# Performance work log

Measured on AMD Instinct MI355X. Metric: run time of the kernel, lower is better.

## Reference

```python
import jax, jax.numpy as jnp
import numpy as np

NHID = 1024
NOUT = 50257
NLAY = 1
MAX_LEN = 24


def setup_inputs() -> dict:
    key = jax.random.key(0)
    ks = jax.random.split(key, 16)
    s = 0.02
    return {
        "inp": jax.random.randint(ks[0], (1,), 0, NOUT),
        "hidden": jax.random.normal(ks[1], (1, 1, NHID), dtype=jnp.float32),
        "encoder_output": jax.random.normal(ks[2], (1, NHID), dtype=jnp.float32),
        "encoder_outputs": jax.random.normal(ks[3], (MAX_LEN, NHID), dtype=jnp.float32),
        "emb_W": jax.random.normal(ks[4], (NOUT, NHID), dtype=jnp.float32) * s,
        "attn_W": jax.random.normal(ks[5], (MAX_LEN, 2 * NHID), dtype=jnp.float32) * s,
        "attn_b": jnp.zeros((MAX_LEN,), dtype=jnp.float32),
        "comb_W": jax.random.normal(ks[6], (NHID, 2 * NHID), dtype=jnp.float32) * s,
        "comb_b": jnp.zeros((NHID,), dtype=jnp.float32),
        "W_ih": jax.random.normal(ks[7], (3 * NHID, NHID), dtype=jnp.float32) * s,
        "W_hh": jax.random.normal(ks[8], (3 * NHID, NHID), dtype=jnp.float32) * s,
        "b_ih": jnp.zeros((3 * NHID,), dtype=jnp.float32),
        "b_hh": jnp.zeros((3 * NHID,), dtype=jnp.float32),
        "out_W": jax.random.normal(ks[9], (NOUT, NHID), dtype=jnp.float32) * s,
        "out_b": jnp.zeros((NOUT,), dtype=jnp.float32),
    }


def reference(inp, hidden, encoder_output, encoder_outputs, emb_W, attn_W, attn_b,
              comb_W, comb_b, W_ih, W_hh, b_ih, b_hh, out_W, out_b):
    # embedding lookup (dropout is identity in eval); [1, nhid]
    embedded = emb_W[inp]
    h = hidden[0]  # [1, nhid]
    # Bahdanau-style attention over encoder_outputs [max_len, nhid]
    attn_in = jnp.concatenate([embedded, h], axis=1)            # [1, 2*nhid]
    attn_weights = jax.nn.softmax(attn_in @ attn_W.T + attn_b, axis=-1)  # [1, max_len]
    attn_applied = attn_weights @ encoder_outputs               # [1, nhid]
    out = jnp.concatenate([embedded, attn_applied], axis=1) @ comb_W.T + comb_b  # [1, nhid]
    # nlay repeated (relu -> GRU step) with the same single-layer GRU weights
    for _ in range(NLAY):
        x = jax.nn.relu(out)
        gi = x @ W_ih.T + b_ih   # [1, 3*nhid]
        gh = h @ W_hh.T + b_hh   # [1, 3*nhid]
        ir, iz, i_n = jnp.split(gi, 3, axis=1)
        hr, hz, h_n = jnp.split(gh, 3, axis=1)
        r = jax.nn.sigmoid(ir + hr)
        z = jax.nn.sigmoid(iz + hz)
        n = jnp.tanh(i_n + r * h_n)
        h = (1.0 - z) * n + z * h
        out = h
    logp = jax.nn.log_softmax(out @ out_W.T + out_b, axis=-1)   # [1, nout]
    return (logp, h[None, :, :], attn_weights)
```

## Files before the change

kernel.cpp:

```cpp
#include <hip/hip_runtime.h>
#include <math.h>

#define NHID 1024
#define NOUT 50257
#define MAXLEN 24

#define WS_APP   0
#define WS_X     1024
#define WS_GH    2048
#define WS_H     5120
#define WS_LOGIT 8192
#define WS_PAIRS 61440

#define LOG_BLOCKS 786

__device__ __forceinline__ float wave_reduce_sum(float v) {
    #pragma unroll
    for (int off = 32; off > 0; off >>= 1) v += __shfl_down(v, off, 64);
    return v;
}

__device__ __forceinline__ void lse_merge(float& m, float& s, float m2, float s2) {
    float M = fmaxf(m, m2);
    s = s * expf(m - M) + s2 * expf(m2 - M);
    m = M;
}

__global__ __launch_bounds__(1024) void
k_attn_gh(const int* __restrict__ inp, const float* __restrict__ hid,
          const float* __restrict__ enc, const float* __restrict__ embW,
          const float* __restrict__ attnW, const float* __restrict__ attnb,
          const float* __restrict__ Whh, const float* __restrict__ bhh,
          float* __restrict__ ws, float* __restrict__ out) {
    const int tid = threadIdx.x;
    const int lane = tid & 63, wave = tid >> 6;
    const float4* hid4 = (const float4*)hid;

    if (blockIdx.x > 0) {
        const int row = (blockIdx.x - 1) * 16 + wave;
        const float4* w4 = (const float4*)(Whh + (size_t)row * NHID);
        float acc = 0.f;
        #pragma unroll
        for (int it = 0; it < 4; ++it) {
            int idx = it * 64 + lane;
            float4 w = w4[idx], h = hid4[idx];
            acc += w.x * h.x + w.y * h.y + w.z * h.z + w.w * h.w;
        }
        acc = wave_reduce_sum(acc);
        if (lane == 0) ws[WS_GH + row] = acc + bhh[row];
        return;
    }

    __shared__ float s_sc[MAXLEN];
    __shared__ float s_w[MAXLEN];
    const float4* emb4 = (const float4*)(embW + (size_t)inp[0] * NHID);
    for (int i = wave; i < MAXLEN; i += 16) {
        const float4* w4 = (const float4*)(attnW + (size_t)i * 2 * NHID);
        float acc = 0.f;
        #pragma unroll
        for (int it = 0; it < 8; ++it) {
            int idx = it * 64 + lane;
            float4 w = w4[idx];
            float4 a = (idx < 256) ? emb4[idx] : hid4[idx - 256];
            acc += w.x * a.x + w.y * a.y + w.z * a.z + w.w * a.w;
        }
        acc = wave_reduce_sum(acc);
        if (lane == 0) s_sc[i] = acc + attnb[i];
    }
    __syncthreads();
    if (tid == 0) {
        float m = -1e30f;
        for (int i = 0; i < MAXLEN; ++i) m = fmaxf(m, s_sc[i]);
        float s = 0.f;
        for (int i = 0; i < MAXLEN; ++i) { float e = expf(s_sc[i] - m); s_w[i] = e; s += e; }
        float inv = 1.f / s;
        for (int i = 0; i < MAXLEN; ++i) { s_w[i] *= inv; out[NOUT + NHID + i] = s_w[i]; }
    }
    __syncthreads();
    {
        float acc = 0.f;
        #pragma unroll 4
        for (int i = 0; i < MAXLEN; ++i) acc += s_w[i] * enc[i * NHID + tid];
        ws[WS_APP + tid] = acc;
    }
}

__global__ __launch_bounds__(256) void
k_comb(const int* __restrict__ inp, const float* __restrict__ embW,
       const float* __restrict__ combW, const float* __restrict__ combb,
       float* __restrict__ ws) {
    const int j = blockIdx.x, t = threadIdx.x;
    const float4* emb4 = (const float4*)(embW + (size_t)inp[0] * NHID);
    const float4* app4 = (const float4*)(ws + WS_APP);
    const float4* w4 = (const float4*)(combW + (size_t)j * 2 * NHID);
    float4 wa = w4[t],       xa = emb4[t];
    float4 wb = w4[256 + t], xb = app4[t];
    float p = wa.x * xa.x + wa.y * xa.y + wa.z * xa.z + wa.w * xa.w
            + wb.x * xb.x + wb.y * xb.y + wb.z * xb.z + wb.w * xb.w;
    p = wave_reduce_sum(p);
    __shared__ float s_r[4];
    if ((t & 63) == 0) s_r[t >> 6] = p;
    __syncthreads();
    if (t == 0) ws[WS_X + j] = fmaxf(s_r[0] + s_r[1] + s_r[2] + s_r[3] + combb[j], 0.f);
}

__global__ __launch_bounds__(256) void
k_gru(const float* __restrict__ hid, const float* __restrict__ Wih,
      const float* __restrict__ bih, float* __restrict__ ws,
      float* __restrict__ out) {
    const int j = blockIdx.x, t = threadIdx.x;
    const float4* x4 = (const float4*)(ws + WS_X);
    float4 xv = x4[t];
    float p[3];
    #pragma unroll
    for (int r = 0; r < 3; ++r) {
        float4 wv = ((const float4*)(Wih + (size_t)(r * NHID + j) * NHID))[t];
        p[r] = wv.x * xv.x + wv.y * xv.y + wv.z * xv.z + wv.w * xv.w;
    }
    __shared__ float s_r[3][4];
    #pragma unroll
    for (int r = 0; r < 3; ++r) {
        float v = wave_reduce_sum(p[r]);
        if ((t & 63) == 0) s_r[r][t >> 6] = v;
    }
    __syncthreads();
    if (t == 0) {
        float gi[3];
        #pragma unroll
        for (int r = 0; r < 3; ++r) gi[r] = s_r[r][0] + s_r[r][1] + s_r[r][2] + s_r[r][3] + bih[r * NHID + j];
        float hr = ws[WS_GH + j], hz = ws[WS_GH + NHID + j], hn = ws[WS_GH + 2 * NHID + j];
        float r_ = 1.f / (1.f + expf(-(gi[0] + hr)));
        float z_ = 1.f / (1.f + expf(-(gi[1] + hz)));
        float n_ = tanhf(gi[2] + r_ * hn);
        float hnew = (1.f - z_) * n_ + z_ * hid[j];
        ws[WS_H + j] = hnew;
        out[NOUT + j] = hnew;
    }
}

__global__ __launch_bounds__(1024) void
k_logits(const float* __restrict__ outW, const float* __restrict__ outb,
         float* __restrict__ ws) {
    const int tid = threadIdx.x;
    const int lane = tid & 63, wave = tid >> 6;
    const float4* h4 = (const float4*)(ws + WS_H);
    float4 hv[4];
    #pragma unroll
    for (int it = 0; it < 4; ++it) hv[it] = h4[it * 64 + lane];
    float m = -1e30f, s = 0.f;
    const int rowBase = blockIdx.x * 64 + wave * 4;
    #pragma unroll
    for (int rr = 0; rr < 4; ++rr) {
        const int row = rowBase + rr;
        if (row >= NOUT) break;
        const float4* w4 = (const float4*)(outW + (size_t)row * NHID);
        float acc = 0.f;
        #pragma unroll
        for (int it = 0; it < 4; ++it) {
            float4 w = w4[it * 64 + lane];
            acc += w.x * hv[it].x + w.y * hv[it].y + w.z * hv[it].z + w.w * hv[it].w;
        }
        acc = wave_reduce_sum(acc);
        if (lane == 0) {
            float v = acc + outb[row];
            ws[WS_LOGIT + row] = v;
            lse_merge(m, s, v, 1.f);
        }
    }
    __shared__ float sm[16], ss[16];
    if (lane == 0) { sm[wave] = m; ss[wave] = s; }
    __syncthreads();
    if (tid == 0) {
        float M = sm[0], S = ss[0];
        #pragma unroll
        for (int w = 1; w < 16; ++w) lse_merge(M, S, sm[w], ss[w]);
        ws[WS_PAIRS + 2 * blockIdx.x] = M;
        ws[WS_PAIRS + 2 * blockIdx.x + 1] = S;
    }
}

__global__ __launch_bounds__(1024) void
k_finalize(const float* __restrict__ ws, float* __restrict__ out) {
    const int tid = threadIdx.x;
    const int lane = tid & 63, wave = tid >> 6;
    float m = -1e30f, s = 0.f;
    if (tid < LOG_BLOCKS) { m = ws[WS_PAIRS + 2 * tid]; s = ws[WS_PAIRS + 2 * tid + 1]; }
    #pragma unroll
    for (int off = 32; off > 0; off >>= 1) {
        float m2 = __shfl_down(m, off, 64);
        float s2 = __shfl_down(s, off, 64);
        lse_merge(m, s, m2, s2);
    }
    __shared__ float sm[16], ss[16];
    __shared__ float sC;
    if (lane == 0) { sm[wave] = m; ss[wave] = s; }
    __syncthreads();
    if (tid == 0) {
        float M = sm[0], S = ss[0];
        #pragma unroll
        for (int w = 1; w < 16; ++w) lse_merge(M, S, sm[w], ss[w]);
        sC = M + logf(S);
    }
    __syncthreads();
    const float C = sC;
    const int i = blockIdx.x * 1024 + tid;
    if (i < NOUT) out[i] = ws[WS_LOGIT + i] - C;
}

extern "C" void kernel_launch(void* const* d_in, const int* in_sizes, int n_in,
                              void* d_out, int out_size, void* d_ws, size_t ws_size,
                              hipStream_t stream) {
    const int*   inp   = (const int*)d_in[0];
    const float* hid   = (const float*)d_in[1];
    const float* enc   = (const float*)d_in[3];
    const float* embW  = (const float*)d_in[4];
    const float* attnW = (const float*)d_in[5];
    const float* attnb = (const float*)d_in[6];
    const float* combW = (const float*)d_in[7];
    const float* combb = (const float*)d_in[8];
    const float* Wih   = (const float*)d_in[9];
    const float* Whh   = (const float*)d_in[10];
    const float* bih   = (const float*)d_in[11];
    const float* bhh   = (const float*)d_in[12];
    const float* outW  = (const float*)d_in[13];
    const float* outb  = (const float*)d_in[14];
    float* out = (float*)d_out;
    float* ws  = (float*)d_ws;

    hipLaunchKernelGGL(k_attn_gh, dim3(1 + 192), dim3(1024), 0, stream,
                       inp, hid, enc, embW, attnW, attnb, Whh, bhh, ws, out);
    hipLaunchKernelGGL(k_comb, dim3(NHID), dim3(256), 0, stream,
                       inp, embW, combW, combb, ws);
    hipLaunchKernelGGL(k_gru, dim3(NHID), dim3(256), 0, stream,
                       hid, Wih, bih, ws, out);
    hipLaunchKernelGGL(k_logits, dim3(LOG_BLOCKS), dim3(1024), 0, stream,
                       outW, outb, ws);
    hipLaunchKernelGGL(k_finalize, dim3(50), dim3(1024), 0, stream,
                       ws, out);
}
```

Baseline: 426.5 us.

## Fuse decoder step into one cooperative persistent kernel with grid syncs

Replaces the five separate kernel launches (attention/gh, combine, GRU, logits, finalize) with a single cooperative kernel of 256 blocks that separates stages with grid-wide syncs. This removes inter-kernel launch gaps and tail effects. The combine and GRU matvecs are remapped to one wave per output row, and the logits stage loops over row groups persistently. The trade-off is fewer resident waves per CU for the bandwidth-bound output projection, plus the cost of grid barriers.

```diff
diff --git a/kernel.cpp b/kernel.cpp
--- a/kernel.cpp
+++ b/kernel.cpp
@@ -1,5 +1,8 @@
 #include <hip/hip_runtime.h>
+#include <hip/hip_cooperative_groups.h>
 #include <math.h>
+
+namespace cg = cooperative_groups;
 
 #define NHID 1024
 #define NOUT 50257
@@ -12,7 +15,8 @@
 #define WS_LOGIT 8192
 #define WS_PAIRS 61440
 
-#define LOG_BLOCKS 786
+#define NBLK 256
+#define NGROUP 786
 
 __device__ __forceinline__ float wave_reduce_sum(float v) {
     #pragma unroll
@@ -27,17 +31,57 @@
 }
 
 __global__ __launch_bounds__(1024) void
-k_attn_gh(const int* __restrict__ inp, const float* __restrict__ hid,
-          const float* __restrict__ enc, const float* __restrict__ embW,
-          const float* __restrict__ attnW, const float* __restrict__ attnb,
-          const float* __restrict__ Whh, const float* __restrict__ bhh,
-          float* __restrict__ ws, float* __restrict__ out) {
+k_fused(const int* __restrict__ inp, const float* __restrict__ hid,
+        const float* __restrict__ enc, const float* __restrict__ embW,
+        const float* __restrict__ attnW, const float* __restrict__ attnb,
+        const float* __restrict__ combW, const float* __restrict__ combb,
+        const float* __restrict__ Wih, const float* __restrict__ Whh,
+        const float* __restrict__ bih, const float* __restrict__ bhh,
+        const float* __restrict__ outW, const float* __restrict__ outb,
+        float* __restrict__ ws, float* __restrict__ out) {
+    cg::grid_group grid = cg::this_grid();
     const int tid = threadIdx.x;
     const int lane = tid & 63, wave = tid >> 6;
+    const int bid = blockIdx.x;
+    const int gwave = bid * 16 + wave;
+
+    __shared__ float s_sc[MAXLEN], s_w[MAXLEN];
+    __shared__ float sm[16], ss[16];
+    __shared__ float sC;
+
     const float4* hid4 = (const float4*)hid;
-
-    if (blockIdx.x > 0) {
-        const int row = (blockIdx.x - 1) * 16 + wave;
+    const float4* emb4 = (const float4*)(embW + (size_t)inp[0] * NHID);
+
+    if (bid == 0) {
+        for (int i = wave; i < MAXLEN; i += 16) {
+            const float4* w4 = (const float4*)(attnW + (size_t)i * 2 * NHID);
+            float acc = 0.f;
+            #pragma unroll
+            for (int it = 0; it < 8; ++it) {
+                int idx = it * 64 + lane;
+                float4 w = w4[idx];
+                float4 a = (idx < 256) ? emb4[idx] : hid4[idx - 256];
+                acc += w.x * a.x + w.y * a.y + w.z * a.z + w.w * a.w;
+            }
+            acc = wave_reduce_sum(acc);
+            if (lane == 0) s_sc[i] = acc + attnb[i];
+        }
+        __syncthreads();
+        if (tid == 0) {
+            float m = -1e30f;
+            for (int i = 0; i < MAXLEN; ++i) m = fmaxf(m, s_sc[i]);
+            float s = 0.f;
+            for (int i = 0; i < MAXLEN; ++i) { float e = expf(s_sc[i] - m); s_w[i] = e; s += e; }
+            float inv = 1.f / s;
+            for (int i = 0; i < MAXLEN; ++i) { s_w[i] *= inv; out[NOUT + NHID + i] = s_w[i]; }
+        }
+        __syncthreads();
+        float acc = 0.f;
+        #pragma unroll 4
+        for (int i = 0; i < MAXLEN; ++i) acc += s_w[i] * enc[i * NHID + tid];
+        ws[WS_APP + tid] = acc;
+    } else if (bid <= 192) {
+        const int row = (bid - 1) * 16 + wave;
         const float4* w4 = (const float4*)(Whh + (size_t)row * NHID);
         float acc = 0.f;
         #pragma unroll
@@ -48,163 +92,119 @@
         }
         acc = wave_reduce_sum(acc);
         if (lane == 0) ws[WS_GH + row] = acc + bhh[row];
-        return;
-    }
-
-    __shared__ float s_sc[MAXLEN];
-    __shared__ float s_w[MAXLEN];
-    const float4* emb4 = (const float4*)(embW + (size_t)inp[0] * NHID);
-    for (int i = wave; i < MAXLEN; i += 16) {
-        const float4* w4 = (const float4*)(attnW + (size_t)i * 2 * NHID);
+    }
+    grid.sync();
+
+    if (gwave < NHID) {
+        const int j = gwave;
+        const float4* app4 = (const float4*)(ws + WS_APP);
+        const float4* w4 = (const float4*)(combW + (size_t)j * 2 * NHID);
         float acc = 0.f;
         #pragma unroll
         for (int it = 0; it < 8; ++it) {
             int idx = it * 64 + lane;
             float4 w = w4[idx];
-            float4 a = (idx < 256) ? emb4[idx] : hid4[idx - 256];
+            float4 a = (idx < 256) ? emb4[idx] : app4[idx - 256];
             acc += w.x * a.x + w.y * a.y + w.z * a.z + w.w * a.w;
         }
         acc = wave_reduce_sum(acc);
-        if (lane == 0) s_sc[i] = acc + attnb[i];
-    }
-    __syncthreads();
-    if (tid == 0) {
-        float m = -1e30f;
-        for (int i = 0; i < MAXLEN; ++i) m = fmaxf(m, s_sc[i]);
-        float s = 0.f;
-        for (int i = 0; i < MAXLEN; ++i) { float e = expf(s_sc[i] - m); s_w[i] = e; s += e; }
-        float inv = 1.f / s;
-        for (int i = 0; i < MAXLEN; ++i) { s_w[i] *= inv; out[NOUT + NHID + i] = s_w[i]; }
+        if (lane == 0) ws[WS_X + j] = fmaxf(acc + combb[j], 0.f);
+    }
+    grid.sync();
+
+    if (gwave < NHID) {
+        const int j = gwave;
+        const float4* x4 = (const float4*)(ws + WS_X);
+        float4 xv[4];
+        #pragma unroll
+        for (int it = 0; it < 4; ++it) xv[it] = x4[it * 64 + lane];
+        float gi[3];
+        #pragma unroll
+        for (int r = 0; r < 3; ++r) {
+            const float4* w4 = (const float4*)(Wih + (size_t)(r * NHID + j) * NHID);
+            float acc = 0.f;
+            #pragma unroll
+            for (int it = 0; it < 4; ++it) {
+                float4 w = w4[it * 64 + lane];
+                acc += w.x * xv[it].x + w.y * xv[it].y + w.z * xv[it].z + w.w * xv[it].w;
+            }
+            gi[r] = wave_reduce_sum(acc);
+        }
+        if (lane == 0) {
+            float ir = gi[0] + bih[j],            hr = ws[WS_GH + j];
+            float iz = gi[1] + bih[NHID + j],     hz = ws[WS_GH + NHID + j];
+            float in_ = gi[2] + bih[2 * NHID + j], hn = ws[WS_GH + 2 * NHID + j];
+            float r_ = 1.f / (1.f + expf(-(ir + hr)));
+            float z_ = 1.f / (1.f + expf(-(iz + hz)));
+            float n_ = tanhf(in_ + r_ * hn);
+            float hnew = (1.f - z_) * n_ + z_ * hid[j];
+            ws[WS_H + j] = hnew;
+            out[NOUT + j] = hnew;
+        }
+    }
+    grid.sync();
+
+    {
+        const float4* h4 = (const float4*)(ws + WS_H);
+        float4 hv[4];
+        #pragma unroll
+        for (int it = 0; it < 4; ++it) hv[it] = h4[it * 64 + lane];
+        float m = -1e30f, s = 0.f;
+        for (int g = bid; g < NGROUP; g += NBLK) {
+            const int rowBase = g * 64 + wave * 4;
+            #pragma unroll
+            for (int rr = 0; rr < 4; ++rr) {
+                const int row = rowBase + rr;
+                if (row < NOUT) {
+                    const float4* w4 = (const float4*)(outW + (size_t)row * NHID);
+                    float acc = 0.f;
+                    #pragma unroll
+                    for (int it = 0; it < 4; ++it) {
+                        float4 w = w4[it * 64 + lane];
+                        acc += w.x * hv[it].x + w.y * hv[it].y + w.z * hv[it].z + w.w * hv[it].w;
+                    }
+                    acc = wave_reduce_sum(acc);
+                    if (lane == 0) {
+                        float v = acc + outb[row];
+                        ws[WS_LOGIT + row] = v;
+                        lse_merge(m, s, v, 1.f);
+                    }
+                }
+            }
+        }
+        if (lane == 0) { sm[wave] = m; ss[wave] = s; }
+        __syncthreads();
+        if (tid == 0) {
+            float M = sm[0], S = ss[0];
+            #pragma unroll
+            for (int w = 1; w < 16; ++w) lse_merge(M, S, sm[w], ss[w]);
+            ws[WS_PAIRS + 2 * bid] = M;
+            ws[WS_PAIRS + 2 * bid + 1] = S;
+        }
+    }
+    grid.sync();
+
+    if (wave == 0) {
+        float m = -1e30f, s = 0.f;
+        #pragma unroll
+        for (int k = 0; k < 4; ++k) {
+            int idx = k * 64 + lane;
+            lse_merge(m, s, ws[WS_PAIRS + 2 * idx], ws[WS_PAIRS + 2 * idx + 1]);
+        }
+        #pragma unroll
+        for (int off = 32; off > 0; off >>= 1) {
+            float m2 = __shfl_down(m, off, 64);
+            float s2 = __shfl_down(s, off, 64);
+            lse_merge(m, s, m2, s2);
+        }
+        if (lane == 0) sC = m + logf(s);
     }
     __syncthreads();
     {
-        float acc = 0.f;
-        #pragma unroll 4
-        for (int i = 0; i < MAXLEN; ++i) acc += s_w[i] * enc[i * NHID + tid];
-        ws[WS_APP + tid] = acc;
-    }
-}
-
-__global__ __launch_bounds__(256) void
-k_comb(const int* __restrict__ inp, const float* __restrict__ embW,
-       const float* __restrict__ combW, const float* __restrict__ combb,
-       float* __restrict__ ws) {
-    const int j = blockIdx.x, t = threadIdx.x;
-    const float4* emb4 = (const float4*)(embW + (size_t)inp[0] * NHID);
-    const float4* app4 = (const float4*)(ws + WS_APP);
-    const float4* w4 = (const float4*)(combW + (size_t)j * 2 * NHID);
-    float4 wa = w4[t],       xa = emb4[t];
-    float4 wb = w4[256 + t], xb = app4[t];
-    float p = wa.x * xa.x + wa.y * xa.y + wa.z * xa.z + wa.w * xa.w
-            + wb.x * xb.x + wb.y * xb.y + wb.z * xb.z + wb.w * xb.w;
-    p = wave_reduce_sum(p);
-    __shared__ float s_r[4];
-    if ((t & 63) == 0) s_r[t >> 6] = p;
-    __syncthreads();
-    if (t == 0) ws[WS_X + j] = fmaxf(s_r[0] + s_r[1] + s_r[2] + s_r[3] + combb[j], 0.f);
-}
-
-__global__ __launch_bounds__(256) void
-k_gru(const float* __restrict__ hid, const float* __restrict__ Wih,
-      const float* __restrict__ bih, float* __restrict__ ws,
-      float* __restrict__ out) {
-    const int j = blockIdx.x, t = threadIdx.x;
-    const float4* x4 = (const float4*)(ws + WS_X);
-    float4 xv = x4[t];
-    float p[3];
-    #pragma unroll
-    for (int r = 0; r < 3; ++r) {
-        float4 wv = ((const float4*)(Wih + (size_t)(r * NHID + j) * NHID))[t];
-        p[r] = wv.x * xv.x + wv.y * xv.y + wv.z * xv.z + wv.w * xv.w;
-    }
-    __shared__ float s_r[3][4];
-    #pragma unroll
-    for (int r = 0; r < 3; ++r) {
-        float v = wave_reduce_sum(p[r]);
-        if ((t & 63) == 0) s_r[r][t >> 6] = v;
-    }
-    __syncthreads();
-    if (t == 0) {
-        float gi[3];
-        #pragma unroll
-        for (int r = 0; r < 3; ++r) gi[r] = s_r[r][0] + s_r[r][1] + s_r[r][2] + s_r[r][3] + bih[r * NHID + j];
-        float hr = ws[WS_GH + j], hz = ws[WS_GH + NHID + j], hn = ws[WS_GH + 2 * NHID + j];
-        float r_ = 1.f / (1.f + expf(-(gi[0] + hr)));
-        float z_ = 1.f / (1.f + expf(-(gi[1] + hz)));
-        float n_ = tanhf(gi[2] + r_ * hn);
-        float hnew = (1.f - z_) * n_ + z_ * hid[j];
-        ws[WS_H + j] = hnew;
-        out[NOUT + j] = hnew;
-    }
-}
-
-__global__ __launch_bounds__(1024) void
-k_logits(const float* __restrict__ outW, const float* __restrict__ outb,
-         float* __restrict__ ws) {
-    const int tid = threadIdx.x;
-    const int lane = tid & 63, wave = tid >> 6;
-    const float4* h4 = (const float4*)(ws + WS_H);
-    float4 hv[4];
-    #pragma unroll
-    for (int it = 0; it < 4; ++it) hv[it] = h4[it * 64 + lane];
-    float m = -1e30f, s = 0.f;
-    const int rowBase = blockIdx.x * 64 + wave * 4;
-    #pragma unroll
-    for (int rr = 0; rr < 4; ++rr) {
-        const int row = rowBase + rr;
-        if (row >= NOUT) break;
-        const float4* w4 = (const float4*)(outW + (size_t)row * NHID);
-        float acc = 0.f;
-        #pragma unroll
-        for (int it = 0; it < 4; ++it) {
-            float4 w = w4[it * 64 + lane];
-            acc += w.x * hv[it].x + w.y * hv[it].y + w.z * hv[it].z + w.w * hv[it].w;
-        }
-        acc = wave_reduce_sum(acc);
-        if (lane == 0) {
-            float v = acc + outb[row];
-            ws[WS_LOGIT + row] = v;
-            lse_merge(m, s, v, 1.f);
-        }
-    }
-    __shared__ float sm[16], ss[16];
-    if (lane == 0) { sm[wave] = m; ss[wave] = s; }
-    __syncthreads();
-    if (tid == 0) {
-        float M = sm[0], S = ss[0];
-        #pragma unroll
-        for (int w = 1; w < 16; ++w) lse_merge(M, S, sm[w], ss[w]);
-        ws[WS_PAIRS + 2 * blockIdx.x] = M;
-        ws[WS_PAIRS + 2 * blockIdx.x + 1] = S;
-    }
-}
-
-__global__ __launch_bounds__(1024) void
-k_finalize(const float* __restrict__ ws, float* __restrict__ out) {
-    const int tid = threadIdx.x;
-    const int lane = tid & 63, wave = tid >> 6;
-    float m = -1e30f, s = 0.f;
-    if (tid < LOG_BLOCKS) { m = ws[WS_PAIRS + 2 * tid]; s = ws[WS_PAIRS + 2 * tid + 1]; }
-    #pragma unroll
-    for (int off = 32; off > 0; off >>= 1) {
-        float m2 = __shfl_down(m, off, 64);
-        float s2 = __shfl_down(s, off, 64);
-        lse_merge(m, s, m2, s2);
-    }
-    __shared__ float sm[16], ss[16];
-    __shared__ float sC;
-    if (lane == 0) { sm[wave] = m; ss[wave] = s; }
-    __syncthreads();
-    if (tid == 0) {
-        float M = sm[0], S = ss[0];
-        #pragma unroll
-        for (int w = 1; w < 16; ++w) lse_merge(M, S, sm[w], ss[w]);
-        sC = M + logf(S);
-    }
-    __syncthreads();
-    const float C = sC;
-    const int i = blockIdx.x * 1024 + tid;
-    if (i < NOUT) out[i] = ws[WS_LOGIT + i] - C;
+        const float C = sC;
+        const int i = bid * 1024 + tid;
+        if (i < NOUT) out[i] = ws[WS_LOGIT + i] - C;
+    }
 }
 
 extern "C" void kernel_launch(void* const* d_in, const int* in_sizes, int n_in,
@@ -227,14 +227,9 @@
     float* out = (float*)d_out;
     float* ws  = (float*)d_ws;
 
-    hipLaunchKernelGGL(k_attn_gh, dim3(1 + 192), dim3(1024), 0, stream,
-                       inp, hid, enc, embW, attnW, attnb, Whh, bhh, ws, out);
-    hipLaunchKernelGGL(k_comb, dim3(NHID), dim3(256), 0, stream,
-                       inp, embW, combW, combb, ws);
-    hipLaunchKernelGGL(k_gru, dim3(NHID), dim3(256), 0, stream,
-                       hid, Wih, bih, ws, out);
-    hipLaunchKernelGGL(k_logits, dim3(LOG_BLOCKS), dim3(1024), 0, stream,
-                       outW, outb, ws);
-    hipLaunchKernelGGL(k_finalize, dim3(50), dim3(1024), 0, stream,
-                       ws, out);
-}
+    void* args[] = { (void*)&inp, (void*)&hid, (void*)&enc, (void*)&embW,
+                     (void*)&attnW, (void*)&attnb, (void*)&combW, (void*)&combb,
+                     (void*)&Wih, (void*)&Whh, (void*)&bih, (void*)&bhh,
+                     (void*)&outW, (void*)&outb, (void*)&ws, (void*)&out };
+    hipLaunchCooperativeKernel((void*)k_fused, dim3(NBLK), dim3(1024), args, 0, stream);
+}
```

Result: slower. 559.6 us (+31.2%).
